# Kernel tuning notes

Hardware: AMD Instinct MI355X
Metric: run time of the kernel (lower is better)

## Reference

```python
import jax, jax.numpy as jnp
import numpy as np
from jax.scipy.special import logsumexp

T = 8192        # trajectory length
S_DIM = 256     # state feature dim
B_OPT = 64      # number of options b
N_ACT = 64      # number of actions
STOP_IX = 0     # STOP_NET_STOP_IX
CONT_IX = 1     # STOP_NET_CONTINUE_IX


def setup_inputs() -> dict:
    key = jax.random.key(0)
    k1, k2, k3, k4, k5 = jax.random.split(key, 5)
    s_i = jax.random.normal(k1, (T + 1, S_DIM), dtype=jnp.float32)
    W_action = jax.random.normal(k2, (S_DIM, B_OPT, N_ACT), dtype=jnp.float32) * 0.02
    W_stop = jax.random.normal(k3, (S_DIM, B_OPT, 2), dtype=jnp.float32) * 0.02
    W_start = jax.random.normal(k4, (S_DIM, B_OPT), dtype=jnp.float32) * 0.02
    actions = jax.random.randint(k5, (T,), 0, N_ACT, dtype=jnp.int32)
    return {"s_i": s_i, "W_action": W_action, "W_stop": W_stop,
            "W_start": W_start, "actions": actions, "lengths": T}


def reference(s_i, W_action, W_stop, W_start, actions, lengths):
    # control_net heads: per-state, per-option log-probabilities
    action_logps = jax.nn.log_softmax(jnp.einsum('ts,sbn->tbn', s_i, W_action), axis=-1)  # (T+1, b, n_act)
    stop_logps = jax.nn.log_softmax(jnp.einsum('ts,sbc->tbc', s_i, W_stop), axis=-1)      # (T+1, b, 2)
    start_logps = jax.nn.log_softmax(jnp.einsum('ts,sb->tb', s_i, W_start), axis=-1)      # (T+1, b)

    Tn = actions.shape[0]
    # emission logp of the taken action at each step: (T, b)
    emit = jnp.take_along_axis(action_logps[:Tn], actions[:, None, None].astype(jnp.int32), axis=2)[:, :, 0]

    f0 = start_logps[0] + emit[0]  # (b,)
    eye = jnp.eye(B_OPT, dtype=bool)
    neg_inf = jnp.float32(-jnp.inf)

    def step(f_prev, xs):
        beta, one_minus_beta, start, em = xs
        # trans[i, j] = logaddexp(beta_i + start_j, delta_ij * log(1-beta_i))
        cont = jnp.where(eye, one_minus_beta[:, None], neg_inf)
        trans = jnp.logaddexp(beta[:, None] + start[None, :], cont)
        f = logsumexp(f_prev[:, None] + trans + em[None, :], axis=0)
        return f, None

    xs = (stop_logps[1:Tn, :, STOP_IX], stop_logps[1:Tn, :, CONT_IX],
          start_logps[1:Tn], emit[1:])
    f, _ = jax.lax.scan(step, f0, xs)

    total_logp = logsumexp(f + stop_logps[Tn, :, STOP_IX])
    return -total_logp
```

## Files before the change

kernel.cpp:

```cpp
#include <hip/hip_runtime.h>
#include <stdint.h>


typedef short bf16x8 __attribute__((ext_vector_type(8)));
typedef float f32x4  __attribute__((ext_vector_type(4)));
typedef unsigned short u16;

#define T_LEN 8192
#define SDIM  256

#define WS_SBF    0
#define WS_WAT    4227072
#define WS_WSMT   6324224
#define WS_PE     6422528
#define WS_PS     8519680
#define WS_PB     10617088
#define WS_PC     12714496
#define WS_MOUT   14811904
#define WS_LSC    16909056
#define WS_GOUT   WS_PC
#define WS_GLSC   (WS_PC + 262144)

__device__ inline u16 f2bf(float f) {
  union { float f; uint32_t u; } v; v.f = f;
  uint32_t u = v.u;
  return (u16)((u + 0x7fffu + ((u >> 16) & 1u)) >> 16);
}

__global__ void conv_all(const float* __restrict__ s_i, const float* __restrict__ Wa,
                         const float* __restrict__ Wstop, const float* __restrict__ Wstart,
                         u16* __restrict__ s_bf, u16* __restrict__ wa_t,
                         u16* __restrict__ wsm_t) {
  const int bid = blockIdx.x;
  const int tid = threadIdx.x;
  if (bid < 8256) {
    int idx = bid * 256 + tid;
    int t = idx >> 8;
    float v = (t < T_LEN + 1) ? s_i[idx] : 0.f;
    s_bf[idx] = f2bf(v);
  } else if (bid < 8256 + 4096) {
    int idx = (bid - 8256) * 256 + tid;
    int s = idx >> 12, bn = idx & 4095;
    wa_t[bn * 256 + s] = f2bf(Wa[idx]);
  } else {
    int idx = (bid - 12352) * 256 + tid;
    int col = idx >> 8, s = idx & 255;
    float v;
    if (col < 64)       v = Wstart[s * 64 + col];
    else if (col < 128) v = Wstop[s * 128 + (col - 64) * 2 + 0];
    else                v = Wstop[s * 128 + (col - 128) * 2 + 1];
    wsm_t[col * 256 + s] = f2bf(v);
  }
}

__global__ __launch_bounds__(256, 4) void gemm_fused(
    const u16* __restrict__ s_bf, const u16* __restrict__ wa_t,
    const u16* __restrict__ wsm_t, const int* __restrict__ actions,
    float* __restrict__ peT, float* __restrict__ ps,
    float* __restrict__ pb, float* __restrict__ pc) {
  __shared__ uint4 ldsU[64 * 32];
  const int tid = threadIdx.x;
  const int lane = tid & 63;
  const int w = tid >> 6;
  const int g = lane >> 4, c = lane & 15;
  const int bid = blockIdx.x;

  if (bid < 129) {
    uint4* sA = ldsU;
    uint4* sB = ldsU + 512;
    const int t0 = bid * 64;

    f32x4 acc[12];
#pragma unroll
    for (int i = 0; i < 12; ++i) acc[i] = (f32x4){0.f, 0.f, 0.f, 0.f};

    for (int kq = 0; kq < 4; ++kq) {
      if (kq) __syncthreads();
#pragma unroll
      for (int i = tid; i < 512; i += 256) {
        int row = i >> 3, u = i & 7;
        sA[row * 8 + (u ^ (row & 7))] =
            *(const uint4*)(s_bf + (size_t)(t0 + row) * 256 + kq * 64 + u * 8);
      }
#pragma unroll
      for (int i = tid; i < 1536; i += 256) {
        int row = i >> 3, u = i & 7;
        sB[row * 8 + (u ^ (row & 7))] =
            *(const uint4*)(wsm_t + (size_t)row * 256 + kq * 64 + u * 8);
      }
      __syncthreads();
#pragma unroll
      for (int kk = 0; kk < 2; ++kk) {
        int u = kk * 4 + g;
        int arow = w * 16 + c;
        bf16x8 af = *(const bf16x8*)&sA[arow * 8 + (u ^ (arow & 7))];
#pragma unroll
        for (int cf = 0; cf < 12; ++cf) {
          int brow = cf * 16 + c;
          bf16x8 bfr = *(const bf16x8*)&sB[brow * 8 + (u ^ (brow & 7))];
          acc[cf] = __builtin_amdgcn_mfma_f32_16x16x32_bf16(af, bfr, acc[cf], 0, 0, 0);
        }
      }
    }

#pragma unroll
    for (int q = 0; q < 4; ++q) {
      int t = t0 + w * 16 + g * 4 + q;
      float v0 = acc[0][q], v1 = acc[1][q], v2 = acc[2][q], v3 = acc[3][q];
      float m = fmaxf(fmaxf(v0, v1), fmaxf(v2, v3));
#pragma unroll
      for (int d = 1; d < 16; d <<= 1) m = fmaxf(m, __shfl_xor(m, d));
      float s = __expf(v0 - m) + __expf(v1 - m) + __expf(v2 - m) + __expf(v3 - m);
#pragma unroll
      for (int d = 1; d < 16; d <<= 1) s += __shfl_xor(s, d);
      float lse = m + __logf(s);
      if (t <= T_LEN) {
        ps[t * 64 + 0 * 16 + c] = __expf(v0 - lse);
        ps[t * 64 + 1 * 16 + c] = __expf(v1 - lse);
        ps[t * 64 + 2 * 16 + c] = __expf(v2 - lse);
        ps[t * 64 + 3 * 16 + c] = __expf(v3 - lse);
#pragma unroll
        for (int bf = 0; bf < 4; ++bf) {
          float l0 = acc[4 + bf][q], l1 = acc[8 + bf][q];
          float d01 = l0 - l1;
          pb[t * 64 + bf * 16 + c] = 1.f / (1.f + __expf(-d01));
          pc[t * 64 + bf * 16 + c] = 1.f / (1.f + __expf(d01));
        }
      }
    }
    return;
  }

  const int abid = bid - 129;
  int swz = (abid & 7) * 512 + (abid >> 3);
  const int t0 = (swz >> 6) * 128;
  const int b0 = swz & 63;
  const int tbase = t0 + w * 32;

  int act[2][4];
#pragma unroll
  for (int mf = 0; mf < 2; ++mf)
#pragma unroll
    for (int q = 0; q < 4; ++q)
      act[mf][q] = actions[tbase + mf * 16 + g * 4 + q];

  const u16* aRow0 = s_bf + (size_t)(tbase + c) * 256;
  const u16* aRow1 = s_bf + (size_t)(tbase + 16 + c) * 256;

  bf16x8 af0[2][4];
#pragma unroll
  for (int ks = 0; ks < 4; ++ks) {
    af0[0][ks] = *(const bf16x8*)(aRow0 + ks * 32 + g * 8);
    af0[1][ks] = *(const bf16x8*)(aRow1 + ks * 32 + g * 8);
  }

  {
    const u16* bsrc = wa_t + (size_t)b0 * 64 * 256;
#pragma unroll
    for (int it = 0; it < 8; ++it) {
      int i = tid + 256 * it;
      int r = i >> 5, s = i & 31;
      ldsU[r * 32 + (s ^ (r & 7))] = *(const uint4*)(bsrc + r * 256 + s * 8);
    }
  }
  __syncthreads();

  f32x4 acc[2][4];
#pragma unroll
  for (int mf = 0; mf < 2; ++mf)
#pragma unroll
    for (int nf = 0; nf < 4; ++nf) acc[mf][nf] = (f32x4){0.f, 0.f, 0.f, 0.f};

  bf16x8 af1[2][4];
#pragma unroll
  for (int ks = 0; ks < 4; ++ks) {
    af1[0][ks] = *(const bf16x8*)(aRow0 + 128 + ks * 32 + g * 8);
    af1[1][ks] = *(const bf16x8*)(aRow1 + 128 + ks * 32 + g * 8);
  }

#pragma unroll
  for (int ks = 0; ks < 4; ++ks) {
#pragma unroll
    for (int nf = 0; nf < 4; ++nf) {
      int rr = nf * 16 + c;
      bf16x8 bfv = *(const bf16x8*)&ldsU[rr * 32 + ((ks * 4 + g) ^ (rr & 7))];
      acc[0][nf] = __builtin_amdgcn_mfma_f32_16x16x32_bf16(af0[0][ks], bfv, acc[0][nf], 0, 0, 0);
      acc[1][nf] = __builtin_amdgcn_mfma_f32_16x16x32_bf16(af0[1][ks], bfv, acc[1][nf], 0, 0, 0);
    }
  }
#pragma unroll
  for (int ks = 0; ks < 4; ++ks) {
#pragma unroll
    for (int nf = 0; nf < 4; ++nf) {
      int rr = nf * 16 + c;
      bf16x8 bfv = *(const bf16x8*)&ldsU[rr * 32 + (((ks + 4) * 4 + g) ^ (rr & 7))];
      acc[0][nf] = __builtin_amdgcn_mfma_f32_16x16x32_bf16(af1[0][ks], bfv, acc[0][nf], 0, 0, 0);
      acc[1][nf] = __builtin_amdgcn_mfma_f32_16x16x32_bf16(af1[1][ks], bfv, acc[1][nf], 0, 0, 0);
    }
  }

  const size_t pebase = (size_t)b0 * 8192;
#pragma unroll
  for (int mf = 0; mf < 2; ++mf) {
#pragma unroll
    for (int q = 0; q < 4; ++q) {
      float e0 = __expf(acc[mf][0][q]);
      float e1 = __expf(acc[mf][1][q]);
      float e2 = __expf(acc[mf][2][q]);
      float e3 = __expf(acc[mf][3][q]);
      float s = (e0 + e1) + (e2 + e3);
#pragma unroll
      for (int d = 1; d < 16; d <<= 1) s += __shfl_xor(s, d);
      int a = act[mf][q];
      int acf = a >> 4;
      float esel = (acf == 0) ? e0 : (acf == 1) ? e1 : (acf == 2) ? e2 : e3;
      if (c == (a & 15))
        peT[pebase + tbase + mf * 16 + g * 4 + q] = esel / s;
    }
  }
}

__global__ __launch_bounds__(256) void chunk_kernel(
    const float* __restrict__ peT, const float* __restrict__ ps,
    const float* __restrict__ pb, const float* __restrict__ pc,
    float* __restrict__ Mout, float* __restrict__ lscale) {
  __shared__ float scal[64 * 196];
  __shared__ float part[2][256];
  __shared__ float mxs[4];
  const int ck = blockIdx.x;
  const int tid = threadIdx.x;
  const int lane = tid & 63;
  const int w = tid >> 6;
  const int tlo = ck * 64 + 1;

#pragma unroll
  for (int it = 0; it < 16; ++it) {
    int i = tid + 256 * it;
    int st = i >> 6, j = i & 63;
    int t = tlo + st;
    if (t <= T_LEN - 1) {
      int base = t * 64 + j;
      scal[st * 196 + j]       = pb[base];
      scal[st * 196 + 64 + j]  = pc[base];
      scal[st * 196 + 128 + j] = ps[base];
    } else {
      scal[st * 196 + j]       = 0.f;
      scal[st * 196 + 64 + j]  = 1.f;
      scal[st * 196 + 128 + j] = 0.f;
    }
  }
  __syncthreads();
#pragma unroll
  for (int it = 0; it < 16; ++it) {
    int i = tid + 256 * it;
    int j = i >> 6, st = i & 63;
    int t = tlo + st;
    if (t <= T_LEN - 1) {
      float e = peT[(size_t)j * 8192 + t];
      scal[st * 196 + 64 + j]  *= e;
      scal[st * 196 + 128 + j] *= e;
    }
  }
  __syncthreads();

  float M[16];
#pragma unroll
  for (int jj = 0; jj < 16; ++jj) M[jj] = ((w * 16 + jj) == lane) ? 1.f : 0.f;
  float lsc = 0.f;
  int pbuf = 0;

  for (int st = 0; st < 64; ++st) {
    const float* sb = &scal[st * 196];
    float p0 = 0.f, p1 = 0.f, p2 = 0.f, p3 = 0.f;
#pragma unroll
    for (int q = 0; q < 4; ++q) {
      float4 bq = *(const float4*)(sb + w * 16 + q * 4);
      p0 = fmaf(bq.x, M[q * 4 + 0], p0);
      p1 = fmaf(bq.y, M[q * 4 + 1], p1);
      p2 = fmaf(bq.z, M[q * 4 + 2], p2);
      p3 = fmaf(bq.w, M[q * 4 + 3], p3);
    }
    part[pbuf][w * 64 + lane] = (p0 + p1) + (p2 + p3);
    __syncthreads();
    float wv = part[pbuf][lane] + part[pbuf][64 + lane] +
               part[pbuf][128 + lane] + part[pbuf][192 + lane];
    pbuf ^= 1;
#pragma unroll
    for (int q = 0; q < 4; ++q) {
      float4 ecq = *(const float4*)(sb + 64 + w * 16 + q * 4);
      float4 esq = *(const float4*)(sb + 128 + w * 16 + q * 4);
      M[q * 4 + 0] = fmaf(ecq.x, M[q * 4 + 0], esq.x * wv);
      M[q * 4 + 1] = fmaf(ecq.y, M[q * 4 + 1], esq.y * wv);
      M[q * 4 + 2] = fmaf(ecq.z, M[q * 4 + 2], esq.z * wv);
      M[q * 4 + 3] = fmaf(ecq.w, M[q * 4 + 3], esq.w * wv);
    }
    if ((st & 7) == 7) {
      float mx = M[0];
#pragma unroll
      for (int jj = 1; jj < 16; ++jj) mx = fmaxf(mx, M[jj]);
#pragma unroll
      for (int d = 1; d < 64; d <<= 1) mx = fmaxf(mx, __shfl_xor(mx, d));
      if (lane == 0) mxs[w] = mx;
      __syncthreads();
      float bm = fmaxf(fmaxf(mxs[0], mxs[1]), fmaxf(mxs[2], mxs[3]));
      float inv = 1.f / bm;
#pragma unroll
      for (int jj = 0; jj < 16; ++jj) M[jj] *= inv;
      lsc += __logf(bm);
    }
  }

  float* out = Mout + (size_t)ck * 4096;
#pragma unroll
  for (int q = 0; q < 4; ++q) {
    float4 v = make_float4(M[q * 4 + 0], M[q * 4 + 1], M[q * 4 + 2], M[q * 4 + 3]);
    *(float4*)(out + lane * 64 + w * 16 + q * 4) = v;
  }
  if (tid == 0) lscale[ck] = lsc;
}

__global__ __launch_bounds__(256) void group_combine(
    const float* __restrict__ Mout, const float* __restrict__ lscale,
    float* __restrict__ Gout, float* __restrict__ glsc) {
  const int g = blockIdx.x;
  const int tid = threadIdx.x;
  const int j = tid & 63;
  const int w = tid >> 6;
  __shared__ float Xa[64 * 68];
  __shared__ float Xb[64 * 68];
  __shared__ float Ma[64 * 68];
  __shared__ float Mb[64 * 68];
  __shared__ float red[4];

  {
    const float* M0 = Mout + (size_t)(8 * g) * 4096;
    const float* M1 = Mout + (size_t)(8 * g + 1) * 4096;
    for (int idx = tid; idx < 4096; idx += 256) {
      int i = idx >> 6, r = idx & 63;
      Xa[r * 68 + i] = M0[idx];
      Ma[i * 68 + r] = M1[idx];
    }
  }
  __syncthreads();

  float lsc = 0.f;
  float* Xcur = Xa; float* Xnxt = Xb;
  float* Mcur = Ma; float* Mnxt = Mb;

  for (int m = 1; m < 8; ++m) {
    float4 pf[4];
    if (m < 7) {
      const float* Mn = Mout + (size_t)(8 * g + m + 1) * 4096;
#pragma unroll
      for (int ii = 0; ii < 4; ++ii)
        pf[ii] = *(const float4*)(Mn + tid * 4 + 1024 * ii);
    }

    float acc[16];
#pragma unroll
    for (int i = 0; i < 16; ++i) acc[i] = 0.f;

#pragma unroll 4
    for (int k = 0; k < 64; ++k) {
      float mv = Mcur[k * 68 + j];
      const float* xr = Xcur + k * 68 + (w << 4);
      float4 x0 = *(const float4*)(xr + 0);
      float4 x1 = *(const float4*)(xr + 4);
      float4 x2 = *(const float4*)(xr + 8);
      float4 x3 = *(const float4*)(xr + 12);
      acc[0]  = fmaf(mv, x0.x, acc[0]);  acc[1]  = fmaf(mv, x0.y, acc[1]);
      acc[2]  = fmaf(mv, x0.z, acc[2]);  acc[3]  = fmaf(mv, x0.w, acc[3]);
      acc[4]  = fmaf(mv, x1.x, acc[4]);  acc[5]  = fmaf(mv, x1.y, acc[5]);
      acc[6]  = fmaf(mv, x1.z, acc[6]);  acc[7]  = fmaf(mv, x1.w, acc[7]);
      acc[8]  = fmaf(mv, x2.x, acc[8]);  acc[9]  = fmaf(mv, x2.y, acc[9]);
      acc[10] = fmaf(mv, x2.z, acc[10]); acc[11] = fmaf(mv, x2.w, acc[11]);
      acc[12] = fmaf(mv, x3.x, acc[12]); acc[13] = fmaf(mv, x3.y, acc[13]);
      acc[14] = fmaf(mv, x3.z, acc[14]); acc[15] = fmaf(mv, x3.w, acc[15]);
    }

    float lm = acc[0];
#pragma unroll
    for (int i = 1; i < 16; ++i) lm = fmaxf(lm, acc[i]);
#pragma unroll
    for (int d = 1; d < 64; d <<= 1) lm = fmaxf(lm, __shfl_xor(lm, d));
    if ((tid & 63) == 0) red[w] = lm;
    __syncthreads();
    float bm = fmaxf(fmaxf(red[0], red[1]), fmaxf(red[2], red[3]));
    float inv = 1.f / bm;
    lsc += __logf(bm);
#pragma unroll
    for (int i = 0; i < 16; ++i)
      Xnxt[j * 68 + (w << 4) + i] = acc[i] * inv;
    if (m < 7) {
#pragma unroll
      for (int ii = 0; ii < 4; ++ii) {
        int idx = tid * 4 + 1024 * ii;
        int k = idx >> 6, jj = idx & 63;
        *(float4*)(Mnxt + k * 68 + jj) = pf[ii];
      }
    }
    __syncthreads();
    float* t = Xcur; Xcur = Xnxt; Xnxt = t;
    float* tm = Mcur; Mcur = Mnxt; Mnxt = tm;
  }

  float* out = Gout + (size_t)g * 4096;
  for (int idx = tid; idx < 4096; idx += 256) {
    int i = idx >> 6, r = idx & 63;
    out[idx] = Xcur[r * 68 + i];
  }
  if (tid == 0) {
    float s = lsc;
#pragma unroll
    for (int m = 0; m < 8; ++m) s += lscale[8 * g + m];
    glsc[g] = s;
  }
}

__global__ __launch_bounds__(256) void final_combine(
    const float* __restrict__ Gout, const float* __restrict__ glsc,
    const float* __restrict__ peT, const float* __restrict__ ps,
    const float* __restrict__ pb, float* __restrict__ out) {
  const int tid = threadIdx.x;
  const int j = tid & 63, w = tid >> 6;
  __shared__ float vsh[64];
  __shared__ float part[4 * 64];
  if (tid < 64) vsh[tid] = ps[tid] * peT[(size_t)tid * 8192];
  __syncthreads();
  double lsc = 0.0;
  for (int gph = 0; gph < 16; ++gph) {
    const float* Gc = Gout + (size_t)gph * 4096;
    const int k0 = w << 4;
    float a0 = 0.f, a1 = 0.f, a2 = 0.f, a3 = 0.f;
#pragma unroll
    for (int kk = 0; kk < 16; kk += 4) {
      a0 = fmaf(vsh[k0 + kk + 0], Gc[(k0 + kk + 0) * 64 + j], a0);
      a1 = fmaf(vsh[k0 + kk + 1], Gc[(k0 + kk + 1) * 64 + j], a1);
      a2 = fmaf(vsh[k0 + kk + 2], Gc[(k0 + kk + 2) * 64 + j], a2);
      a3 = fmaf(vsh[k0 + kk + 3], Gc[(k0 + kk + 3) * 64 + j], a3);
    }
    part[w * 64 + j] = (a0 + a1) + (a2 + a3);
    __syncthreads();
    if (w == 0) {
      float u = part[j] + part[64 + j] + part[128 + j] + part[192 + j];
      float mx = u;
#pragma unroll
      for (int d = 1; d < 64; d <<= 1) mx = fmaxf(mx, __shfl_xor(mx, d));
      vsh[j] = u / mx;
      lsc += (double)__logf(mx) + (double)glsc[gph];
    }
    __syncthreads();
  }
  if (w == 0) {
    float z = vsh[j] * pb[T_LEN * 64 + j];
#pragma unroll
    for (int d = 1; d < 64; d <<= 1) z += __shfl_xor(z, d);
    if (j == 0) out[0] = (float)(-((double)logf(z) + lsc));
  }
}

extern "C" void kernel_launch(void* const* d_in, const int* in_sizes, int n_in,
                              void* d_out, int out_size, void* d_ws, size_t ws_size,
                              hipStream_t stream) {
  const float* s_i      = (const float*)d_in[0];
  const float* W_action = (const float*)d_in[1];
  const float* W_stop   = (const float*)d_in[2];
  const float* W_start  = (const float*)d_in[3];
  const int*   actions  = (const int*)d_in[4];

  char* ws = (char*)d_ws;
  u16*   s_bf  = (u16*)(ws + WS_SBF);
  u16*   wa_t  = (u16*)(ws + WS_WAT);
  u16*   wsm_t = (u16*)(ws + WS_WSMT);
  float* peT   = (float*)(ws + WS_PE);
  float* ps    = (float*)(ws + WS_PS);
  float* pb    = (float*)(ws + WS_PB);
  float* pc    = (float*)(ws + WS_PC);
  float* Mout  = (float*)(ws + WS_MOUT);
  float* lsc   = (float*)(ws + WS_LSC);
  float* Gout  = (float*)(ws + WS_GOUT);
  float* glsc  = (float*)(ws + WS_GLSC);

  conv_all<<<12544, 256, 0, stream>>>(s_i, W_action, W_stop, W_start, s_bf, wa_t, wsm_t);
  gemm_fused<<<4225, 256, 0, stream>>>(s_bf, wa_t, wsm_t, actions, peT, ps, pb, pc);
  chunk_kernel<<<128, 256, 0, stream>>>(peT, ps, pb, pc, Mout, lsc);
  group_combine<<<16, 256, 0, stream>>>(Mout, lsc, Gout, glsc);
  final_combine<<<1, 256, 0, stream>>>(Gout, glsc, peT, ps, pb, (float*)d_out);
}
```

Measured before the change: 135.9 us.

## Remap chunk recurrence so row reductions stay within lane quads

The per-step matrix recurrence in chunk_kernel is re-partitioned so that each group of four adjacent lanes holds one full 64-element row of M. The dot product can then be reduced with two xor shuffles instead of a shared-memory partial-sum exchange. This removes the __syncthreads at every time step and leaves only the one at each 8-step renormalization. The cost is more LDS reads, since every lane loads its own 16-wide slices of b, e and s. The output write indexing is changed to match the new layout.

```diff
diff --git a/kernel.cpp b/kernel.cpp
--- a/kernel.cpp
+++ b/kernel.cpp
@@ -225,7 +225,6 @@
     const float* __restrict__ pb, const float* __restrict__ pc,
     float* __restrict__ Mout, float* __restrict__ lscale) {
   __shared__ float scal[64 * 196];
-  __shared__ float part[2][256];
   __shared__ float mxs[4];
   const int ck = blockIdx.x;
   const int tid = threadIdx.x;
@@ -263,59 +262,71 @@
   }
   __syncthreads();
 
+  const int kcol = w * 16 + (lane >> 2);
+  const int roff = (lane & 3) * 16;
+
   float M[16];
 #pragma unroll
-  for (int jj = 0; jj < 16; ++jj) M[jj] = ((w * 16 + jj) == lane) ? 1.f : 0.f;
+  for (int jj = 0; jj < 16; ++jj) M[jj] = ((roff + jj) == kcol) ? 1.f : 0.f;
   float lsc = 0.f;
-  int pbuf = 0;
-
-  for (int st = 0; st < 64; ++st) {
-    const float* sb = &scal[st * 196];
-    float p0 = 0.f, p1 = 0.f, p2 = 0.f, p3 = 0.f;
-#pragma unroll
-    for (int q = 0; q < 4; ++q) {
-      float4 bq = *(const float4*)(sb + w * 16 + q * 4);
-      p0 = fmaf(bq.x, M[q * 4 + 0], p0);
-      p1 = fmaf(bq.y, M[q * 4 + 1], p1);
-      p2 = fmaf(bq.z, M[q * 4 + 2], p2);
-      p3 = fmaf(bq.w, M[q * 4 + 3], p3);
-    }
-    part[pbuf][w * 64 + lane] = (p0 + p1) + (p2 + p3);
+
+  for (int st8 = 0; st8 < 8; ++st8) {
+#pragma unroll
+    for (int s8 = 0; s8 < 8; ++s8) {
+      const float* sb = &scal[(st8 * 8 + s8) * 196];
+      float4 b0 = *(const float4*)(sb + roff + 0);
+      float4 b1 = *(const float4*)(sb + roff + 4);
+      float4 b2 = *(const float4*)(sb + roff + 8);
+      float4 b3 = *(const float4*)(sb + roff + 12);
+      float p0 = 0.f, p1 = 0.f, p2 = 0.f, p3 = 0.f;
+      p0 = fmaf(b0.x, M[0], p0);  p1 = fmaf(b0.y, M[1], p1);
+      p2 = fmaf(b0.z, M[2], p2);  p3 = fmaf(b0.w, M[3], p3);
+      p0 = fmaf(b1.x, M[4], p0);  p1 = fmaf(b1.y, M[5], p1);
+      p2 = fmaf(b1.z, M[6], p2);  p3 = fmaf(b1.w, M[7], p3);
+      p0 = fmaf(b2.x, M[8], p0);  p1 = fmaf(b2.y, M[9], p1);
+      p2 = fmaf(b2.z, M[10], p2); p3 = fmaf(b2.w, M[11], p3);
+      p0 = fmaf(b3.x, M[12], p0); p1 = fmaf(b3.y, M[13], p1);
+      p2 = fmaf(b3.z, M[14], p2); p3 = fmaf(b3.w, M[15], p3);
+      float p = (p0 + p1) + (p2 + p3);
+      p += __shfl_xor(p, 1);
+      p += __shfl_xor(p, 2);
+      float4 e0 = *(const float4*)(sb + 64 + roff + 0);
+      float4 e1 = *(const float4*)(sb + 64 + roff + 4);
+      float4 e2 = *(const float4*)(sb + 64 + roff + 8);
+      float4 e3 = *(const float4*)(sb + 64 + roff + 12);
+      float4 s0 = *(const float4*)(sb + 128 + roff + 0);
+      float4 s1 = *(const float4*)(sb + 128 + roff + 4);
+      float4 s2 = *(const float4*)(sb + 128 + roff + 8);
+      float4 s3 = *(const float4*)(sb + 128 + roff + 12);
+      M[0]  = fmaf(e0.x, M[0],  s0.x * p);  M[1]  = fmaf(e0.y, M[1],  s0.y * p);
+      M[2]  = fmaf(e0.z, M[2],  s0.z * p);  M[3]  = fmaf(e0.w, M[3],  s0.w * p);
+      M[4]  = fmaf(e1.x, M[4],  s1.x * p);  M[5]  = fmaf(e1.y, M[5],  s1.y * p);
+      M[6]  = fmaf(e1.z, M[6],  s1.z * p);  M[7]  = fmaf(e1.w, M[7],  s1.w * p);
+      M[8]  = fmaf(e2.x, M[8],  s2.x * p);  M[9]  = fmaf(e2.y, M[9],  s2.y * p);
+      M[10] = fmaf(e2.z, M[10], s2.z * p);  M[11] = fmaf(e2.w, M[11], s2.w * p);
+      M[12] = fmaf(e3.x, M[12], s3.x * p);  M[13] = fmaf(e3.y, M[13], s3.y * p);
+      M[14] = fmaf(e3.z, M[14], s3.z * p);  M[15] = fmaf(e3.w, M[15], s3.w * p);
+    }
+    float mx = M[0];
+#pragma unroll
+    for (int jj = 1; jj < 16; ++jj) mx = fmaxf(mx, M[jj]);
+#pragma unroll
+    for (int d = 1; d < 64; d <<= 1) mx = fmaxf(mx, __shfl_xor(mx, d));
+    if (lane == 0) mxs[w] = mx;
     __syncthreads();
-    float wv = part[pbuf][lane] + part[pbuf][64 + lane] +
-               part[pbuf][128 + lane] + part[pbuf][192 + lane];
-    pbuf ^= 1;
-#pragma unroll
-    for (int q = 0; q < 4; ++q) {
-      float4 ecq = *(const float4*)(sb + 64 + w * 16 + q * 4);
-      float4 esq = *(const float4*)(sb + 128 + w * 16 + q * 4);
-      M[q * 4 + 0] = fmaf(ecq.x, M[q * 4 + 0], esq.x * wv);
-      M[q * 4 + 1] = fmaf(ecq.y, M[q * 4 + 1], esq.y * wv);
-      M[q * 4 + 2] = fmaf(ecq.z, M[q * 4 + 2], esq.z * wv);
-      M[q * 4 + 3] = fmaf(ecq.w, M[q * 4 + 3], esq.w * wv);
-    }
-    if ((st & 7) == 7) {
-      float mx = M[0];
-#pragma unroll
-      for (int jj = 1; jj < 16; ++jj) mx = fmaxf(mx, M[jj]);
-#pragma unroll
-      for (int d = 1; d < 64; d <<= 1) mx = fmaxf(mx, __shfl_xor(mx, d));
-      if (lane == 0) mxs[w] = mx;
-      __syncthreads();
-      float bm = fmaxf(fmaxf(mxs[0], mxs[1]), fmaxf(mxs[2], mxs[3]));
-      float inv = 1.f / bm;
-#pragma unroll
-      for (int jj = 0; jj < 16; ++jj) M[jj] *= inv;
-      lsc += __logf(bm);
-    }
-  }
-
-  float* out = Mout + (size_t)ck * 4096;
-#pragma unroll
-  for (int q = 0; q < 4; ++q) {
-    float4 v = make_float4(M[q * 4 + 0], M[q * 4 + 1], M[q * 4 + 2], M[q * 4 + 3]);
-    *(float4*)(out + lane * 64 + w * 16 + q * 4) = v;
-  }
+    float bm = fmaxf(fmaxf(mxs[0], mxs[1]), fmaxf(mxs[2], mxs[3]));
+    float inv = 1.f / bm;
+#pragma unroll
+    for (int jj = 0; jj < 16; ++jj) M[jj] *= inv;
+    lsc += __logf(bm);
+    __syncthreads();
+  }
+
+  float* out = Mout + (size_t)ck * 4096 + kcol * 64 + roff;
+  *(float4*)(out + 0)  = make_float4(M[0],  M[1],  M[2],  M[3]);
+  *(float4*)(out + 4)  = make_float4(M[4],  M[5],  M[6],  M[7]);
+  *(float4*)(out + 8)  = make_float4(M[8],  M[9],  M[10], M[11]);
+  *(float4*)(out + 12) = make_float4(M[12], M[13], M[14], M[15]);
   if (tid == 0) lscale[ck] = lsc;
 }
 
```

After: 131.0 us. 3.5% less time.
